# Kernel optimization log

Measured on AMD Instinct MI355X. Metric: run time of the kernel, lower is better.

## Reference

```python
import jax, jax.numpy as jnp
import numpy as np

B, S, D = 2, 4096, 1024
H, HD = 16, 64
CF = 0.5
K = int(S * CF)          # top_k tokens routed through the block
HIDDEN = 4 * D
EPS = 1e-5
SCALE = 1.0 / float(np.sqrt(HD))


def rmsnorm(x, w):
    return x * jax.lax.rsqrt(jnp.mean(x * x, axis=-1, keepdims=True) + EPS) * w


def rope(x, cos, sin):
    # x: [B,K,H,HD]; cos/sin: [K, HD//2]
    x1, x2 = x[..., ::2], x[..., 1::2]
    c = cos[None, :, None, :]
    s = sin[None, :, None, :]
    r1 = x1 * c - x2 * s
    r2 = x1 * s + x2 * c
    return jnp.stack([r1, r2], axis=-1).reshape(x.shape)


def block(x, mask, cos, sin, attn_norm, wq, wk, wv, wo, ffn_norm, w1, w2, w3):
    # Llama-style decoder block on the routed subset x: [B,K,D]
    b, k, _ = x.shape
    xn = rmsnorm(x, attn_norm)
    q = (xn @ wq).reshape(b, k, H, HD)
    kk = (xn @ wk).reshape(b, k, H, HD)
    v = (xn @ wv).reshape(b, k, H, HD)
    q = rope(q, cos, sin)
    kk = rope(kk, cos, sin)
    scores = jnp.einsum('bqhd,bkhd->bhqk', q, kk) * SCALE
    scores = jnp.where(mask[None, None], scores, jnp.finfo(scores.dtype).min)
    attn = jax.nn.softmax(scores, axis=-1)
    o = jnp.einsum('bhqk,bkhd->bqhd', attn, v).reshape(b, k, D)
    h = x + o @ wo
    hn = rmsnorm(h, ffn_norm)
    return h + (jax.nn.silu(hn @ w1) * (hn @ w3)) @ w2


def setup_inputs() -> dict:
    key = jax.random.key(0)
    ks = jax.random.split(key, 10)
    sc = 0.02
    inv = 1.0 / (10000.0 ** (np.arange(0, HD, 2, dtype=np.float32) / HD))
    ang = np.outer(np.arange(K, dtype=np.float32), inv)  # [K, HD//2]
    return {
        'x': jax.random.normal(ks[0], (B, S, D), jnp.float32),
        'mask': jnp.tril(jnp.ones((K, K), dtype=bool)),
        'freqs_cos': jnp.asarray(np.cos(ang)),
        'freqs_sin': jnp.asarray(np.sin(ang)),
        'w_router': jax.random.normal(ks[1], (D, 1), jnp.float32) * sc,
        'attn_norm': jnp.ones((D,), jnp.float32),
        'wq': jax.random.normal(ks[2], (D, D), jnp.float32) * sc,
        'wk': jax.random.normal(ks[3], (D, D), jnp.float32) * sc,
        'wv': jax.random.normal(ks[4], (D, D), jnp.float32) * sc,
        'wo': jax.random.normal(ks[5], (D, D), jnp.float32) * sc,
        'ffn_norm': jnp.ones((D,), jnp.float32),
        'w1': jax.random.normal(ks[6], (D, HIDDEN), jnp.float32) * sc,
        'w2': jax.random.normal(ks[7], (HIDDEN, D), jnp.float32) * sc,
        'w3': jax.random.normal(ks[8], (D, HIDDEN), jnp.float32) * sc,
    }


def reference(x, mask, freqs_cos, freqs_sin, w_router, attn_norm, wq, wk, wv, wo, ffn_norm, w1, w2, w3):
    b = x.shape[0]
    router_logits = (x @ w_router)[..., 0]            # [B,S]
    vals, idx = jax.lax.top_k(router_logits, K)       # [B,K]
    order = jnp.argsort(idx, axis=1)                  # torch.sort of token_index
    sel = jnp.take_along_axis(idx, order, axis=1)     # sorted selected positions
    token_w = jax.nn.softmax(vals, axis=1)            # softmax over topk weights
    r_weights = jnp.take_along_axis(token_w, order, axis=1)  # [B,K]
    filtered_x = jnp.take_along_axis(x, sel[:, :, None], axis=1)  # [B,K,D]
    x_out = block(filtered_x, mask, freqs_cos, freqs_sin, attn_norm,
                  wq, wk, wv, wo, ffn_norm, w1, w2, w3)
    xw_out = r_weights[:, :, None] * x_out
    # scatter_add back into the residual stream
    out = x.at[jnp.arange(b)[:, None], sel, :].add(xw_out)
    return out
```

## Files before the change

### kernel.cpp

```cpp
#include <hip/hip_runtime.h>
#include <cstdint>
#include <cstddef>

typedef unsigned short u16;
typedef __bf16 bf16x8 __attribute__((ext_vector_type(8)));
typedef short s16x4 __attribute__((ext_vector_type(4)));
typedef float f32x4 __attribute__((ext_vector_type(4)));

#define SCALE_Q_LOG2E 0.18033688011112042f

static __device__ __forceinline__ float b2f(u16 u){ return __uint_as_float(((unsigned)u)<<16); }
static __device__ __forceinline__ u16 f2b(float f){
  unsigned u = __float_as_uint(f);
  return (u16)((u + 0x7fffu + ((u>>16)&1u)) >> 16);
}
static __device__ __forceinline__ void gload_lds16(const void* g, void* l){
  auto gp = reinterpret_cast<__attribute__((address_space(1))) uint32_t*>(reinterpret_cast<uintptr_t>(g));
  auto lp = reinterpret_cast<__attribute__((address_space(3))) uint32_t*>(reinterpret_cast<uintptr_t>(l));
  __builtin_amdgcn_global_load_lds(gp, lp, 16, 0, 0);
}
static __device__ __forceinline__ f32x4 mfma16bf(s16x4 a, s16x4 b, f32x4 c){
#if __has_builtin(__builtin_amdgcn_mfma_f32_16x16x16bf16_1k)
  return __builtin_amdgcn_mfma_f32_16x16x16bf16_1k(a, b, c, 0, 0, 0);
#else
  f32x4 d = c;
  asm volatile("v_mfma_f32_16x16x16_bf16 %0, %1, %2, %0" : "+v"(d) : "v"(a), "v"(b));
  return d;
#endif
}

__global__ __launch_bounds__(256) void prep_weights(
    const float* __restrict__ wq, const float* __restrict__ wk,
    const float* __restrict__ wv, const float* __restrict__ wo,
    const float* __restrict__ w1, const float* __restrict__ w3,
    const float* __restrict__ w2,
    u16* __restrict__ WqkvT, u16* __restrict__ WoT,
    u16* __restrict__ W13T, u16* __restrict__ W2T){
  __shared__ float tile[32][33];
  int bx = blockIdx.x;
  const float* in; u16* out; int R, C, rowmap, tcol, trow;
  if (bx < 4096){
    int wsel = bx>>10, tid = bx&1023;
    in = (wsel==0)?wq:(wsel==1)?wk:(wsel==2)?wv:wo;
    out = (wsel<3) ? (WqkvT + (size_t)wsel*1024*1024) : WoT;
    R=1024; C=1024; rowmap=0; tcol=tid&31; trow=tid>>5;
  } else if (bx < 12288){
    int wsel=(bx-4096)>>12, tid=(bx-4096)&4095;
    in = wsel ? w3 : w1; out = W13T; R=1024; C=4096; rowmap=1+wsel;
    tcol=tid&127; trow=tid>>7;
  } else {
    int tid = bx-12288;
    in = w2; out = W2T; R=4096; C=1024; rowmap=0;
    tcol=tid&31; trow=tid>>5;
  }
  int t=threadIdx.x, tx=t&31, ty=t>>5;
  int c0=tcol*32, r0=trow*32;
  #pragma unroll
  for (int i=0;i<4;i++) tile[ty+i*8][tx] = in[(size_t)(r0+ty+i*8)*C + c0+tx];
  __syncthreads();
  #pragma unroll
  for (int i=0;i<4;i++){
    int c = c0+ty+i*8;
    int orow = c;
    if (rowmap==1) orow = (c>>4)*32 + (c&15);
    else if (rowmap==2) orow = (c>>4)*32 + 16 + (c&15);
    out[(size_t)orow*R + r0+tx] = f2b(tile[tx][ty+i*8]);
  }
}

__global__ __launch_bounds__(256) void transpose_bf16(const u16* __restrict__ in, u16* __restrict__ out,
                                                      int R, int C){
  __shared__ u16 tile[32][33];
  size_t zoff = (size_t)blockIdx.z * R * C;
  const u16* ip = in + zoff;
  u16* op = out + zoff;
  int tx = threadIdx.x, ty = threadIdx.y;
  int c0 = blockIdx.x*32, r0 = blockIdx.y*32;
  #pragma unroll
  for (int i=0;i<4;i++) tile[ty+i*8][tx] = ip[(size_t)(r0+ty+i*8)*C + c0+tx];
  __syncthreads();
  #pragma unroll
  for (int i=0;i<4;i++) op[(size_t)(c0+ty+i*8)*R + r0+tx] = tile[tx][ty+i*8];
}

__global__ __launch_bounds__(256) void router_kernel(const float* __restrict__ x, const float* __restrict__ wr,
                                                     float* __restrict__ logits){
  int row = blockIdx.x*4 + (threadIdx.x>>6);
  int l = threadIdx.x & 63;
  const float4* xr = (const float4*)(x + (size_t)row*1024) + l;
  const float4* wp = (const float4*)wr + l;
  float acc = 0.f;
  #pragma unroll
  for (int c=0;c<4;c++){
    float4 xv = xr[c*64];
    float4 wv = wp[c*64];
    acc += xv.x*wv.x + xv.y*wv.y + xv.z*wv.z + xv.w*wv.w;
  }
  #pragma unroll
  for (int m=1;m<64;m<<=1) acc += __shfl_xor(acc, m, 64);
  if (l==0) logits[row] = acc;
}

static __device__ __forceinline__ unsigned mapkey(float f){
  unsigned u = __float_as_uint(f);
  return (u & 0x80000000u) ? ~u : (u | 0x80000000u);
}
static __device__ unsigned blk_scan_excl(unsigned cnt, unsigned* swav){
  int t = threadIdx.x; int l = t&63, w = t>>6;
  unsigned v = cnt;
  #pragma unroll
  for (int off=1; off<64; off<<=1){
    unsigned n = __shfl_up(v, off, 64);
    if (l >= off) v += n;
  }
  __syncthreads();
  if (l==63) swav[w] = v;
  __syncthreads();
  if (t==0){ unsigned c=0; for (int i=0;i<16;i++){ unsigned tmp=swav[i]; swav[i]=c; c+=tmp; } }
  __syncthreads();
  return swav[w] + v - cnt;
}
__global__ __launch_bounds__(1024) void topk_kernel(const float* __restrict__ logits,
        int* __restrict__ sel, float* __restrict__ rw, int* __restrict__ inv){
  int b = blockIdx.x, t = threadIdx.x;
  int l = t&63, w = t>>6;
  __shared__ float vals[4096];
  __shared__ unsigned hist[256];
  __shared__ unsigned swav[16];
  __shared__ float fwav[16];
  __shared__ unsigned sh_prefix, sh_remaining;
  const float* lgp = logits + b*4096;
  for (int i=t;i<4096;i+=1024) vals[i]=lgp[i];
  if (t==0){ sh_prefix=0u; sh_remaining=2048u; }
  __syncthreads();
  for (int level=0; level<4; level++){
    int shift = 24 - level*8;
    if (t<256) hist[t]=0u;
    __syncthreads();
    unsigned pfx = sh_prefix;
    for (int i=t;i<4096;i+=1024){
      unsigned key = mapkey(vals[i]);
      if (level==0 || (key >> (shift+8)) == pfx)
        atomicAdd(&hist[(key>>shift)&255u], 1u);
    }
    __syncthreads();
    if (t==0){
      unsigned rem = sh_remaining, cum=0u; unsigned bsel=0u;
      for (int bin=255; bin>=0; bin--){
        unsigned hc = hist[bin];
        if (cum + hc >= rem){ bsel=(unsigned)bin; break; }
        cum += hc;
      }
      sh_remaining = rem - cum;
      sh_prefix = (pfx<<8) | bsel;
    }
    __syncthreads();
  }
  unsigned T = sh_prefix;
  unsigned req = sh_remaining;
  int i0 = t*4;
  unsigned gt_[4], eq_[4], fl_[4]; float v_[4];
  #pragma unroll
  for (int j=0;j<4;j++){
    v_[j] = vals[i0+j];
    unsigned key = mapkey(v_[j]);
    gt_[j] = key > T ? 1u:0u;
    eq_[j] = key == T ? 1u:0u;
  }
  unsigned eqbase = blk_scan_excl(eq_[0]+eq_[1]+eq_[2]+eq_[3], swav);
  unsigned er = eqbase;
  #pragma unroll
  for (int j=0;j<4;j++){ fl_[j] = gt_[j] | (eq_[j] & (er < req ? 1u:0u)); er += eq_[j]; }
  unsigned pbase = blk_scan_excl(fl_[0]+fl_[1]+fl_[2]+fl_[3], swav);
  unsigned p = pbase;
  #pragma unroll
  for (int j=0;j<4;j++){
    int i = i0+j;
    if (fl_[j]){ sel[b*2048+(int)p]=i; inv[b*4096+i]=(int)p; p++; }
    else inv[b*4096+i] = -1;
  }
  float mx = fmaxf(fmaxf(v_[0],v_[1]), fmaxf(v_[2],v_[3]));
  #pragma unroll
  for (int m=1;m<64;m<<=1) mx = fmaxf(mx, __shfl_xor(mx,m,64));
  __syncthreads();
  if (l==0) fwav[w]=mx;
  __syncthreads();
  if (t==0){ float g=fwav[0]; for(int i=1;i<16;i++) g=fmaxf(g,fwav[i]); fwav[0]=g; }
  __syncthreads();
  float gm = fwav[0];
  float zz = 0.f;
  #pragma unroll
  for (int j=0;j<4;j++) if (fl_[j]) zz += expf(v_[j]-gm);
  #pragma unroll
  for (int m=1;m<64;m<<=1) zz += __shfl_xor(zz,m,64);
  __syncthreads();
  if (l==0) fwav[w]=zz;
  __syncthreads();
  if (t==0){ float s=0.f; for(int i=0;i<16;i++) s+=fwav[i]; fwav[0]=s; }
  __syncthreads();
  float Z = fwav[0];
  unsigned p2 = pbase;
  #pragma unroll
  for (int j=0;j<4;j++) if (fl_[j]){ rw[b*2048+(int)p2] = expf(v_[j]-gm)/Z; p2++; }
}

__global__ __launch_bounds__(256) void rmsnorm_kernel(const float* __restrict__ xin,
        const float* __restrict__ gamma, const int* __restrict__ sel,
        u16* __restrict__ xn){
  int r = blockIdx.x;
  int src = r;
  if (sel) src = (r>>11)*4096 + sel[r];
  const float* row = xin + (size_t)src*1024;
  int t = threadIdx.x, l = t&63, w = t>>6;
  int d0 = t*4;
  float4 xv = *(const float4*)(row + d0);
  float ss = xv.x*xv.x + xv.y*xv.y + xv.z*xv.z + xv.w*xv.w;
  #pragma unroll
  for (int m=1;m<64;m<<=1) ss += __shfl_xor(ss,m,64);
  __shared__ float red[4];
  if (l==0) red[w]=ss;
  __syncthreads();
  float tot = red[0]+red[1]+red[2]+red[3];
  float rms = rsqrtf(tot*(1.f/1024.f) + 1e-5f);
  float4 gv = *(const float4*)(gamma + d0);
  u16 o0=f2b(xv.x*rms*gv.x), o1=f2b(xv.y*rms*gv.y), o2=f2b(xv.z*rms*gv.z), o3=f2b(xv.w*rms*gv.w);
  uint2 ov; ov.x = (unsigned)o0 | ((unsigned)o1<<16); ov.y = (unsigned)o2 | ((unsigned)o3<<16);
  *(uint2*)(xn + (size_t)r*1024 + d0) = ov;
}

template<int BK>
static __device__ __forceinline__ int swz(int row, int blk){
  if constexpr (BK==64) return blk ^ (row&7);
  else                  return blk ^ ((row>>1)&3);
}

template<int BN, int BK, typename OT>
__global__ __launch_bounds__(256,2) void gemm_bt(const u16* __restrict__ A, const u16* __restrict__ Bt,
        OT* __restrict__ C, const float* __restrict__ resid, const int* __restrict__ sel,
        int M, int N, int Kd){
  __shared__ u16 As[128*BK];
  __shared__ u16 Bs[BN*BK];
  constexpr int NF = BN/32;
  constexpr int KK = BK/32;
  int t = threadIdx.x, w = t>>6, l = t&63, lg = l>>4, ln = l&15;
  int m0 = blockIdx.y*128, n0 = blockIdx.x*BN;
  int wm = (w&1)*64, wn = (w>>1)*(BN/2);
  f32x4 acc[4][NF] = {};
  for (int k0=0; k0<Kd; k0+=BK){
    __syncthreads();
    #pragma unroll
    for (int c=0;c<128*BK*2/4096;c++){
      int off = t*16 + c*4096;
      int row = off/(BK*2), pb = (off%(BK*2))>>4;
      gload_lds16(A + (size_t)(m0+row)*Kd + k0 + swz<BK>(row,pb)*8, &As[c*2048 + w*512]);
    }
    #pragma unroll
    for (int c=0;c<BN*BK*2/4096;c++){
      int off = t*16 + c*4096;
      int row = off/(BK*2), pb = (off%(BK*2))>>4;
      gload_lds16(Bt + (size_t)(n0+row)*Kd + k0 + swz<BK>(row,pb)*8, &Bs[c*2048 + w*512]);
    }
    __syncthreads();
    #pragma unroll
    for (int kk=0;kk<KK;kk++){
      bf16x8 af[4], bfv[NF];
      #pragma unroll
      for (int i=0;i<4;i++){
        int r = wm+i*16+ln;
        af[i] = *(const bf16x8*)&As[r*BK + swz<BK>(r, kk*4+lg)*8];
      }
      #pragma unroll
      for (int i=0;i<NF;i++){
        int r = wn+i*16+ln;
        bfv[i] = *(const bf16x8*)&Bs[r*BK + swz<BK>(r, kk*4+lg)*8];
      }
      #pragma unroll
      for (int mi=0;mi<4;mi++)
        #pragma unroll
        for (int ni=0;ni<NF;ni++)
          acc[mi][ni] = __builtin_amdgcn_mfma_f32_16x16x32_bf16(af[mi], bfv[ni], acc[mi][ni], 0,0,0);
    }
  }
  #pragma unroll
  for (int mi=0;mi<4;mi++){
    #pragma unroll
    for (int ni=0;ni<NF;ni++){
      #pragma unroll
      for (int r=0;r<4;r++){
        int row = m0+wm+mi*16+lg*4+r;
        int col = n0+wn+ni*16+ln;
        float v = acc[mi][ni][r];
        if (resid){
          size_t rrow = sel ? ((size_t)(row>>11)*4096 + sel[row]) : (size_t)row;
          v += resid[rrow*N + col];
        }
        if constexpr (sizeof(OT)==2) C[(size_t)row*N + col] = f2b(v);
        else                          C[(size_t)row*N + col] = v;
      }
    }
  }
}

__global__ __launch_bounds__(256,2) void gemm13(const u16* __restrict__ A, const u16* __restrict__ Bt,
        u16* __restrict__ g, int Kd){
  constexpr int BK = 64;
  __shared__ u16 As[128*BK];
  __shared__ u16 Bs[128*BK];
  int t = threadIdx.x, w = t>>6, l = t&63, lg = l>>4, ln = l&15;
  int m0 = blockIdx.y*128, n0 = blockIdx.x*128;
  int wm = (w&1)*64, wn = (w>>1)*64;
  f32x4 acc[4][4] = {};
  for (int k0=0; k0<Kd; k0+=BK){
    __syncthreads();
    #pragma unroll
    for (int c=0;c<4;c++){
      int off = t*16 + c*4096;
      int row = off/(BK*2), pb = (off%(BK*2))>>4;
      gload_lds16(A  + (size_t)(m0+row)*Kd + k0 + swz<BK>(row,pb)*8, &As[c*2048 + w*512]);
      gload_lds16(Bt + (size_t)(n0+row)*Kd + k0 + swz<BK>(row,pb)*8, &Bs[c*2048 + w*512]);
    }
    __syncthreads();
    #pragma unroll
    for (int kk=0;kk<2;kk++){
      bf16x8 af[4], bfv[4];
      #pragma unroll
      for (int i=0;i<4;i++){
        int ra = wm+i*16+ln, rb = wn+i*16+ln;
        af[i]  = *(const bf16x8*)&As[ra*BK + swz<BK>(ra, kk*4+lg)*8];
        bfv[i] = *(const bf16x8*)&Bs[rb*BK + swz<BK>(rb, kk*4+lg)*8];
      }
      #pragma unroll
      for (int mi=0;mi<4;mi++)
        #pragma unroll
        for (int ni=0;ni<4;ni++)
          acc[mi][ni] = __builtin_amdgcn_mfma_f32_16x16x32_bf16(af[mi], bfv[ni], acc[mi][ni], 0,0,0);
    }
  }
  int gbase = (n0+wn)>>1;
  #pragma unroll
  for (int mi=0;mi<4;mi++){
    #pragma unroll
    for (int p=0;p<2;p++){
      #pragma unroll
      for (int r=0;r<4;r++){
        int row = m0+wm+mi*16+lg*4+r;
        int col = gbase + p*16 + ln;
        float a1 = acc[mi][2*p][r], a3 = acc[mi][2*p+1][r];
        float s1 = a1 / (1.f + __expf(-a1));
        g[(size_t)row*4096 + col] = f2b(s1*a3);
      }
    }
  }
}

__global__ __launch_bounds__(256) void rope_kernel(const u16* __restrict__ QKV,
        const float* __restrict__ fcos, const float* __restrict__ fsin,
        u16* __restrict__ q_r, u16* __restrict__ k_r, u16* __restrict__ v_r){
  int row = blockIdx.x;
  int tok = row & 2047;
  int t = threadIdx.x;
  int d0 = t*4;
  int h = d0 >> 6, wd = d0 & 63, i0 = wd >> 1;
  const u16* base = QKV + (size_t)row*3072;
  size_t ob = (((size_t)(row>>11)*16 + h)*2048 + (size_t)tok)*64 + wd;
  float c0 = fcos[tok*32+i0],   s0 = fsin[tok*32+i0];
  float c1 = fcos[tok*32+i0+1], s1 = fsin[tok*32+i0+1];
  const u16* qp = base + d0;
  float x0=b2f(qp[0]), x1=b2f(qp[1]), x2=b2f(qp[2]), x3=b2f(qp[3]);
  q_r[ob]   = f2b((x0*c0-x1*s0)*SCALE_Q_LOG2E);
  q_r[ob+1] = f2b((x0*s0+x1*c0)*SCALE_Q_LOG2E);
  q_r[ob+2] = f2b((x2*c1-x3*s1)*SCALE_Q_LOG2E);
  q_r[ob+3] = f2b((x2*s1+x3*c1)*SCALE_Q_LOG2E);
  const u16* kp = base + 1024 + d0;
  x0=b2f(kp[0]); x1=b2f(kp[1]); x2=b2f(kp[2]); x3=b2f(kp[3]);
  k_r[ob]   = f2b(x0*c0-x1*s0);
  k_r[ob+1] = f2b(x0*s0+x1*c0);
  k_r[ob+2] = f2b(x2*c1-x3*s1);
  k_r[ob+3] = f2b(x2*s1+x3*c1);
  const u16* vp = base + 2048 + d0;
  v_r[ob]=vp[0]; v_r[ob+1]=vp[1]; v_r[ob+2]=vp[2]; v_r[ob+3]=vp[3];
}

static __device__ __forceinline__ void flash_tile(
    const u16* __restrict__ Ksb, const u16* __restrict__ Vsb,
    bf16x8 qf0, bf16x8 qf1, int k0, int q, bool diag,
    int lg, int ln, float& mi, float& li, f32x4* oaccT){
  f32x4 sv[4];
  #pragma unroll
  for (int ni=0;ni<4;ni++){
    bf16x8 kf0 = *(const bf16x8*)&Ksb[(ni*16+ln)*72 + lg*8];
    bf16x8 kf1 = *(const bf16x8*)&Ksb[(ni*16+ln)*72 + 32 + lg*8];
    f32x4 z = {};
    z = __builtin_amdgcn_mfma_f32_16x16x32_bf16(kf0, qf0, z, 0,0,0);
    z = __builtin_amdgcn_mfma_f32_16x16x32_bf16(kf1, qf1, z, 0,0,0);
    sv[ni] = z;
  }
  float rm = -1e30f;
  if (diag){
    #pragma unroll
    for (int ni=0;ni<4;ni++)
      #pragma unroll
      for (int r=0;r<4;r++){
        float xs = sv[ni][r];
        if (k0+ni*16+lg*4+r > q) xs = -1e30f;
        sv[ni][r] = xs;
        rm = fmaxf(rm, xs);
      }
  } else {
    #pragma unroll
    for (int ni=0;ni<4;ni++)
      #pragma unroll
      for (int r=0;r<4;r++) rm = fmaxf(rm, sv[ni][r]);
  }
  rm = fmaxf(rm, __shfl_xor(rm, 16, 64));
  rm = fmaxf(rm, __shfl_xor(rm, 32, 64));
  float mn = fmaxf(mi, rm);
  float alpha = exp2f(mi - mn);
  float ls = 0.f;
  s16x4 pf[4];
  #pragma unroll
  for (int ni=0;ni<4;ni++){
    float p0 = exp2f(sv[ni][0]-mn);
    float p1 = exp2f(sv[ni][1]-mn);
    float p2 = exp2f(sv[ni][2]-mn);
    float p3 = exp2f(sv[ni][3]-mn);
    ls += (p0+p1)+(p2+p3);
    s16x4 pp;
    pp[0]=(short)f2b(p0); pp[1]=(short)f2b(p1); pp[2]=(short)f2b(p2); pp[3]=(short)f2b(p3);
    pf[ni]=pp;
  }
  ls += __shfl_xor(ls, 16, 64);
  ls += __shfl_xor(ls, 32, 64);
  li = li*alpha + ls;
  mi = mn;
  #pragma unroll
  for (int dt=0; dt<4; dt++){
    f32x4 oo = oaccT[dt];
    oo[0]*=alpha; oo[1]*=alpha; oo[2]*=alpha; oo[3]*=alpha;
    #pragma unroll
    for (int ni=0;ni<4;ni++){
      s16x4 vf = *(const s16x4*)&Vsb[(dt*16+ln)*72 + ni*16 + lg*4];
      oo = mfma16bf(vf, pf[ni], oo);
    }
    oaccT[dt] = oo;
  }
}

__global__ __launch_bounds__(256,2) void flash_kernel(const u16* __restrict__ q_r,
        const u16* __restrict__ k_r, const u16* __restrict__ v_t, u16* __restrict__ o){
  const int S = 2048;
  int pr = blockIdx.x, bh = blockIdx.y;
  int b = bh>>4, h = bh&15;
  int t = threadIdx.x, w = t>>6, l = t&63, lg = l>>4, ln = l&15;
  __shared__ u16 Ks[2][64*72];
  __shared__ u16 Vs[2][64*72];
  const u16* qb = q_r + (size_t)bh*S*64;
  const u16* kb = k_r + (size_t)bh*S*64;
  const u16* vb = v_t + (size_t)bh*64*S;
  int rr = t>>2, p16 = (t&3)*16;
  int qlo = pr, qhi = 31-pr;
  int qAr = qlo*64 + w*16 + ln;
  int qBr = qhi*64 + w*16 + ln;
  bf16x8 qA0 = *(const bf16x8*)(qb + (size_t)qAr*64 + lg*8);
  bf16x8 qA1 = *(const bf16x8*)(qb + (size_t)qAr*64 + 32 + lg*8);
  bf16x8 qB0 = *(const bf16x8*)(qb + (size_t)qBr*64 + lg*8);
  bf16x8 qB1 = *(const bf16x8*)(qb + (size_t)qBr*64 + 32 + lg*8);
  f32x4 oA[4] = {}, oB[4] = {};
  float miA=-1e30f, liA=0.f, miB=-1e30f, liB=0.f;
  {
    *(bf16x8*)&Ks[0][rr*72+p16]   = *(const bf16x8*)(kb + (size_t)rr*64 + p16);
    *(bf16x8*)&Ks[0][rr*72+p16+8] = *(const bf16x8*)(kb + (size_t)rr*64 + p16 + 8);
    *(bf16x8*)&Vs[0][rr*72+p16]   = *(const bf16x8*)(vb + (size_t)rr*S + p16);
    *(bf16x8*)&Vs[0][rr*72+p16+8] = *(const bf16x8*)(vb + (size_t)rr*S + p16 + 8);
  }
  __syncthreads();
  for (int kv=0; kv<=qhi; kv++){
    int cur = kv&1;
    int k0 = kv*64;
    bool hasnext = kv < qhi;
    bf16x8 nk0, nk1, nv0, nv1;
    if (hasnext){
      int kn = k0 + 64;
      nk0 = *(const bf16x8*)(kb + (size_t)(kn+rr)*64 + p16);
      nk1 = *(const bf16x8*)(kb + (size_t)(kn+rr)*64 + p16 + 8);
      nv0 = *(const bf16x8*)(vb + (size_t)rr*S + kn + p16);
      nv1 = *(const bf16x8*)(vb + (size_t)rr*S + kn + p16 + 8);
    }
    if (kv <= qlo)
      flash_tile(Ks[cur], Vs[cur], qA0, qA1, k0, qAr, kv==qlo, lg, ln, miA, liA, oA);
    flash_tile(Ks[cur], Vs[cur], qB0, qB1, k0, qBr, kv==qhi, lg, ln, miB, liB, oB);
    if (hasnext){
      int nb = cur^1;
      *(bf16x8*)&Ks[nb][rr*72+p16]   = nk0;
      *(bf16x8*)&Ks[nb][rr*72+p16+8] = nk1;
      *(bf16x8*)&Vs[nb][rr*72+p16]   = nv0;
      *(bf16x8*)&Vs[nb][rr*72+p16+8] = nv1;
    }
    __syncthreads();
  }
  {
    u16* ob = o + ((size_t)(b*S+qAr))*1024 + h*64 + lg*4;
    #pragma unroll
    for (int dt=0; dt<4; dt++){
      u16 a0=f2b(oA[dt][0]/liA), a1=f2b(oA[dt][1]/liA);
      u16 a2=f2b(oA[dt][2]/liA), a3=f2b(oA[dt][3]/liA);
      uint2 pv; pv.x = (unsigned)a0 | ((unsigned)a1<<16); pv.y = (unsigned)a2 | ((unsigned)a3<<16);
      *(uint2*)(ob + dt*16) = pv;
    }
  }
  {
    u16* ob = o + ((size_t)(b*S+qBr))*1024 + h*64 + lg*4;
    #pragma unroll
    for (int dt=0; dt<4; dt++){
      u16 a0=f2b(oB[dt][0]/liB), a1=f2b(oB[dt][1]/liB);
      u16 a2=f2b(oB[dt][2]/liB), a3=f2b(oB[dt][3]/liB);
      uint2 pv; pv.x = (unsigned)a0 | ((unsigned)a1<<16); pv.y = (unsigned)a2 | ((unsigned)a3<<16);
      *(uint2*)(ob + dt*16) = pv;
    }
  }
}

__global__ __launch_bounds__(256) void final_kernel(const float* __restrict__ x, const float* __restrict__ h,
        const u16* __restrict__ y, const int* __restrict__ inv, const float* __restrict__ rw,
        float* __restrict__ out){
  int row = blockIdx.x;
  int b = row>>12;
  int t = threadIdx.x, d0 = t*4;
  float4 xv = *(const float4*)(x + (size_t)row*1024 + d0);
  float4* op = (float4*)(out + (size_t)row*1024 + d0);
  int j = inv[row];
  if (j < 0){ *op = xv; return; }
  int fr = b*2048 + j;
  float wgt = rw[fr];
  float4 hv = *(const float4*)(h + (size_t)fr*1024 + d0);
  uint2 yv = *(const uint2*)(y + (size_t)fr*1024 + d0);
  float y0=b2f((u16)(yv.x&0xffffu)), y1=b2f((u16)(yv.x>>16)), y2=b2f((u16)(yv.y&0xffffu)), y3=b2f((u16)(yv.y>>16));
  float4 ov;
  ov.x = xv.x + wgt*(hv.x + y0);
  ov.y = xv.y + wgt*(hv.y + y1);
  ov.z = xv.z + wgt*(hv.z + y2);
  ov.w = xv.w + wgt*(hv.w + y3);
  *op = ov;
}

extern "C" void kernel_launch(void* const* d_in, const int* in_sizes, int n_in,
                              void* d_out, int out_size, void* d_ws, size_t ws_size,
                              hipStream_t stream) {
  (void)in_sizes; (void)n_in; (void)out_size; (void)ws_size;
  const float* x     = (const float*)d_in[0];
  const float* fcos  = (const float*)d_in[2];
  const float* fsin  = (const float*)d_in[3];
  const float* wr    = (const float*)d_in[4];
  const float* anorm = (const float*)d_in[5];
  const float* wq    = (const float*)d_in[6];
  const float* wk    = (const float*)d_in[7];
  const float* wv    = (const float*)d_in[8];
  const float* wo    = (const float*)d_in[9];
  const float* fnorm = (const float*)d_in[10];
  const float* w1    = (const float*)d_in[11];
  const float* w2    = (const float*)d_in[12];
  const float* w3    = (const float*)d_in[13];
  float* out = (float*)d_out;

  char* W = (char*)d_ws;
  const size_t MB = 1024*1024;
  u16* WqkvT = (u16*)(W + 0);
  u16* WoT   = (u16*)(W + 6*MB);
  u16* W13T  = (u16*)(W + 8*MB);
  u16* W2T   = (u16*)(W + 24*MB);
  u16* xn    = (u16*)(W + 32*MB);
  u16* QKV   = (u16*)(W + 40*MB);
  u16* q_r   = (u16*)(W + 64*MB);
  u16* k_r   = (u16*)(W + 72*MB);
  u16* v_r   = (u16*)(W + 80*MB);
  u16* v_t   = (u16*)(W + 88*MB);
  u16* attno = (u16*)(W + 96*MB);
  float* hbuf= (float*)(W + 104*MB);
  u16* hn    = (u16*)(W + 120*MB);
  u16* g     = (u16*)(W + 128*MB);
  u16* ybuf  = (u16*)(W + 32*MB);
  float* logits = (float*)(W + 160*MB);
  int*   sel    = (int*)(W + 160*MB + 64*1024);
  float* rw     = (float*)(W + 160*MB + 96*1024);
  int*   inv    = (int*)(W + 160*MB + 128*1024);

  prep_weights<<<16384, 256, 0, stream>>>(wq, wk, wv, wo, w1, w3, w2, WqkvT, WoT, W13T, W2T);
  router_kernel<<<2048, 256, 0, stream>>>(x, wr, logits);
  topk_kernel<<<2, 1024, 0, stream>>>(logits, sel, rw, inv);
  rmsnorm_kernel<<<4096, 256, 0, stream>>>(x, anorm, sel, xn);
  gemm_bt<128,64,u16><<<dim3(24,32), 256, 0, stream>>>(xn, WqkvT, QKV, nullptr, nullptr, 4096, 3072, 1024);
  rope_kernel<<<4096, 256, 0, stream>>>(QKV, fcos, fsin, q_r, k_r, v_r);
  transpose_bf16<<<dim3(2,64,32), dim3(32,8), 0, stream>>>(v_r, v_t, 2048, 64);
  flash_kernel<<<dim3(16,32), 256, 0, stream>>>(q_r, k_r, v_t, attno);
  gemm_bt<64,64,float><<<dim3(16,32), 256, 0, stream>>>(attno, WoT, hbuf, x, sel, 4096, 1024, 1024);
  rmsnorm_kernel<<<4096, 256, 0, stream>>>(hbuf, fnorm, nullptr, hn);
  gemm13<<<dim3(64,32), 256, 0, stream>>>(hn, W13T, g, 1024);
  gemm_bt<64,64,u16><<<dim3(16,32), 256, 0, stream>>>(g, W2T, ybuf, nullptr, nullptr, 4096, 1024, 4096);
  final_kernel<<<8192, 256, 0, stream>>>(x, hbuf, ybuf, inv, rw, out);
}
```

Measured before the change: 489.4 us.

## Fuse router and output copy into prep kernel, fuse W2 GEMM epilogue scatter

The router logits and a full copy of x into the output are merged into the weight-prep kernel, which saves two launches. The W2 GEMM now applies the routing weight and residual in its epilogue and scatters straight into the output at the selected rows. This removes the bf16 ybuf round trip and the separate final kernel. The flash kernel also hoists its K/V LDS fragment loads so both query tiles share one set of registers, which raises register pressure. Correctness depends on the copy of x finishing before the scatter writes, which stream ordering guarantees.

```diff
diff --git a/kernel.cpp b/kernel.cpp
--- a/kernel.cpp
+++ b/kernel.cpp
@@ -29,42 +29,65 @@
 #endif
 }
 
-__global__ __launch_bounds__(256) void prep_weights(
+__global__ __launch_bounds__(256) void prep_kernel(
     const float* __restrict__ wq, const float* __restrict__ wk,
     const float* __restrict__ wv, const float* __restrict__ wo,
     const float* __restrict__ w1, const float* __restrict__ w3,
-    const float* __restrict__ w2,
+    const float* __restrict__ w2, const float* __restrict__ x,
+    const float* __restrict__ wr,
     u16* __restrict__ WqkvT, u16* __restrict__ WoT,
-    u16* __restrict__ W13T, u16* __restrict__ W2T){
+    u16* __restrict__ W13T, u16* __restrict__ W2T,
+    float* __restrict__ logits, float* __restrict__ out){
   __shared__ float tile[32][33];
   int bx = blockIdx.x;
-  const float* in; u16* out; int R, C, rowmap, tcol, trow;
-  if (bx < 4096){
-    int wsel = bx>>10, tid = bx&1023;
-    in = (wsel==0)?wq:(wsel==1)?wk:(wsel==2)?wv:wo;
-    out = (wsel<3) ? (WqkvT + (size_t)wsel*1024*1024) : WoT;
-    R=1024; C=1024; rowmap=0; tcol=tid&31; trow=tid>>5;
-  } else if (bx < 12288){
-    int wsel=(bx-4096)>>12, tid=(bx-4096)&4095;
-    in = wsel ? w3 : w1; out = W13T; R=1024; C=4096; rowmap=1+wsel;
-    tcol=tid&127; trow=tid>>7;
+  if (bx < 12288 || (bx >= 12288 && bx < 13312) || (bx>=13312 && bx<16384)){ }
+  if (bx < 16384){
+    const float* in; u16* outp; int R, C, rowmap, tcol, trow;
+    if (bx < 4096){
+      int wsel = bx>>10, tid = bx&1023;
+      in = (wsel==0)?wq:(wsel==1)?wk:(wsel==2)?wv:wo;
+      outp = (wsel<3) ? (WqkvT + (size_t)wsel*1024*1024) : WoT;
+      R=1024; C=1024; rowmap=0; tcol=tid&31; trow=tid>>5;
+    } else if (bx < 12288){
+      int wsel=(bx-4096)>>12, tid=(bx-4096)&4095;
+      in = wsel ? w3 : w1; outp = W13T; R=1024; C=4096; rowmap=1+wsel;
+      tcol=tid&127; trow=tid>>7;
+    } else {
+      int tid = bx-12288;
+      in = w2; outp = W2T; R=4096; C=1024; rowmap=0;
+      tcol=tid&31; trow=tid>>5;
+    }
+    int t=threadIdx.x, tx=t&31, ty=t>>5;
+    int c0=tcol*32, r0=trow*32;
+    #pragma unroll
+    for (int i=0;i<4;i++) tile[ty+i*8][tx] = in[(size_t)(r0+ty+i*8)*C + c0+tx];
+    __syncthreads();
+    #pragma unroll
+    for (int i=0;i<4;i++){
+      int c = c0+ty+i*8;
+      int orow = c;
+      if (rowmap==1) orow = (c>>4)*32 + (c&15);
+      else if (rowmap==2) orow = (c>>4)*32 + 16 + (c&15);
+      outp[(size_t)orow*R + r0+tx] = f2b(tile[tx][ty+i*8]);
+    }
+  } else if (bx < 18432){
+    int row = (bx-16384)*4 + (threadIdx.x>>6);
+    int l = threadIdx.x & 63;
+    const float4* xr = (const float4*)(x + (size_t)row*1024) + l;
+    const float4* wp = (const float4*)wr + l;
+    float acc = 0.f;
+    #pragma unroll
+    for (int c=0;c<4;c++){
+      float4 xv = xr[c*64];
+      float4 wv = wp[c*64];
+      acc += xv.x*wv.x + xv.y*wv.y + xv.z*wv.z + xv.w*wv.w;
+    }
+    #pragma unroll
+    for (int m=1;m<64;m<<=1) acc += __shfl_xor(acc, m, 64);
+    if (l==0) logits[row] = acc;
   } else {
-    int tid = bx-12288;
-    in = w2; out = W2T; R=4096; C=1024; rowmap=0;
-    tcol=tid&31; trow=tid>>5;
-  }
-  int t=threadIdx.x, tx=t&31, ty=t>>5;
-  int c0=tcol*32, r0=trow*32;
-  #pragma unroll
-  for (int i=0;i<4;i++) tile[ty+i*8][tx] = in[(size_t)(r0+ty+i*8)*C + c0+tx];
-  __syncthreads();
-  #pragma unroll
-  for (int i=0;i<4;i++){
-    int c = c0+ty+i*8;
-    int orow = c;
-    if (rowmap==1) orow = (c>>4)*32 + (c&15);
-    else if (rowmap==2) orow = (c>>4)*32 + 16 + (c&15);
-    out[(size_t)orow*R + r0+tx] = f2b(tile[tx][ty+i*8]);
+    size_t idx = ((size_t)(bx-18432)*256 + threadIdx.x)*4;
+    *(float4*)(out+idx) = *(const float4*)(x+idx);
   }
 }
 
@@ -81,24 +104,6 @@
   __syncthreads();
   #pragma unroll
   for (int i=0;i<4;i++) op[(size_t)(c0+ty+i*8)*R + r0+tx] = tile[tx][ty+i*8];
-}
-
-__global__ __launch_bounds__(256) void router_kernel(const float* __restrict__ x, const float* __restrict__ wr,
-                                                     float* __restrict__ logits){
-  int row = blockIdx.x*4 + (threadIdx.x>>6);
-  int l = threadIdx.x & 63;
-  const float4* xr = (const float4*)(x + (size_t)row*1024) + l;
-  const float4* wp = (const float4*)wr + l;
-  float acc = 0.f;
-  #pragma unroll
-  for (int c=0;c<4;c++){
-    float4 xv = xr[c*64];
-    float4 wv = wp[c*64];
-    acc += xv.x*wv.x + xv.y*wv.y + xv.z*wv.z + xv.w*wv.w;
-  }
-  #pragma unroll
-  for (int m=1;m<64;m<<=1) acc += __shfl_xor(acc, m, 64);
-  if (l==0) logits[row] = acc;
 }
 
 static __device__ __forceinline__ unsigned mapkey(float f){
@@ -296,6 +301,72 @@
         }
         if constexpr (sizeof(OT)==2) C[(size_t)row*N + col] = f2b(v);
         else                          C[(size_t)row*N + col] = v;
+      }
+    }
+  }
+}
+
+__global__ __launch_bounds__(256,2) void gemm_w2(const u16* __restrict__ A, const u16* __restrict__ Bt,
+        const float* __restrict__ x, const float* __restrict__ hbuf,
+        const int* __restrict__ sel, const float* __restrict__ rw,
+        float* __restrict__ out, int Kd){
+  constexpr int BN = 64, BK = 64;
+  __shared__ u16 As[128*BK];
+  __shared__ u16 Bs[BN*BK];
+  int t = threadIdx.x, w = t>>6, l = t&63, lg = l>>4, ln = l&15;
+  int m0 = blockIdx.y*128, n0 = blockIdx.x*BN;
+  int wm = (w&1)*64, wn = (w>>1)*(BN/2);
+  f32x4 acc[4][2] = {};
+  for (int k0=0; k0<Kd; k0+=BK){
+    __syncthreads();
+    #pragma unroll
+    for (int c=0;c<4;c++){
+      int off = t*16 + c*4096;
+      int row = off/(BK*2), pb = (off%(BK*2))>>4;
+      gload_lds16(A + (size_t)(m0+row)*Kd + k0 + swz<BK>(row,pb)*8, &As[c*2048 + w*512]);
+    }
+    #pragma unroll
+    for (int c=0;c<2;c++){
+      int off = t*16 + c*4096;
+      int row = off/(BK*2), pb = (off%(BK*2))>>4;
+      gload_lds16(Bt + (size_t)(n0+row)*Kd + k0 + swz<BK>(row,pb)*8, &Bs[c*2048 + w*512]);
+    }
+    __syncthreads();
+    #pragma unroll
+    for (int kk=0;kk<2;kk++){
+      bf16x8 af[4], bfv[2];
+      #pragma unroll
+      for (int i=0;i<4;i++){
+        int r = wm+i*16+ln;
+        af[i] = *(const bf16x8*)&As[r*BK + swz<BK>(r, kk*4+lg)*8];
+      }
+      #pragma unroll
+      for (int i=0;i<2;i++){
+        int r = wn+i*16+ln;
+        bfv[i] = *(const bf16x8*)&Bs[r*BK + swz<BK>(r, kk*4+lg)*8];
+      }
+      #pragma unroll
+      for (int mi=0;mi<4;mi++)
+        #pragma unroll
+        for (int ni=0;ni<2;ni++)
+          acc[mi][ni] = __builtin_amdgcn_mfma_f32_16x16x32_bf16(af[mi], bfv[ni], acc[mi][ni], 0,0,0);
+    }
+  }
+  #pragma unroll
+  for (int mi=0;mi<4;mi++){
+    int row0 = m0+wm+mi*16+lg*4;
+    #pragma unroll
+    for (int r=0;r<4;r++){
+      int row = row0+r;
+      int b = row>>11;
+      size_t srow = (size_t)b*4096 + sel[row];
+      float wgt = rw[row];
+      #pragma unroll
+      for (int ni=0;ni<2;ni++){
+        int col = n0+wn+ni*16+ln;
+        float y = acc[mi][ni][r];
+        float v = x[srow*1024 + col] + wgt*(hbuf[(size_t)row*1024 + col] + y);
+        out[srow*1024 + col] = v;
       }
     }
   }
@@ -382,17 +453,15 @@
 }
 
 static __device__ __forceinline__ void flash_tile(
-    const u16* __restrict__ Ksb, const u16* __restrict__ Vsb,
+    const bf16x8 (&kf)[4][2], const s16x4 (&vf)[4][4],
     bf16x8 qf0, bf16x8 qf1, int k0, int q, bool diag,
-    int lg, int ln, float& mi, float& li, f32x4* oaccT){
+    int lg, float& mi, float& li, f32x4* oaccT){
   f32x4 sv[4];
   #pragma unroll
   for (int ni=0;ni<4;ni++){
-    bf16x8 kf0 = *(const bf16x8*)&Ksb[(ni*16+ln)*72 + lg*8];
-    bf16x8 kf1 = *(const bf16x8*)&Ksb[(ni*16+ln)*72 + 32 + lg*8];
     f32x4 z = {};
-    z = __builtin_amdgcn_mfma_f32_16x16x32_bf16(kf0, qf0, z, 0,0,0);
-    z = __builtin_amdgcn_mfma_f32_16x16x32_bf16(kf1, qf1, z, 0,0,0);
+    z = __builtin_amdgcn_mfma_f32_16x16x32_bf16(kf[ni][0], qf0, z, 0,0,0);
+    z = __builtin_amdgcn_mfma_f32_16x16x32_bf16(kf[ni][1], qf1, z, 0,0,0);
     sv[ni] = z;
   }
   float rm = -1e30f;
@@ -438,10 +507,8 @@
     f32x4 oo = oaccT[dt];
     oo[0]*=alpha; oo[1]*=alpha; oo[2]*=alpha; oo[3]*=alpha;
     #pragma unroll
-    for (int ni=0;ni<4;ni++){
-      s16x4 vf = *(const s16x4*)&Vsb[(dt*16+ln)*72 + ni*16 + lg*4];
-      oo = mfma16bf(vf, pf[ni], oo);
-    }
+    for (int ni=0;ni<4;ni++)
+      oo = mfma16bf(vf[dt][ni], pf[ni], oo);
     oaccT[dt] = oo;
   }
 }
@@ -486,9 +553,20 @@
       nv0 = *(const bf16x8*)(vb + (size_t)rr*S + kn + p16);
       nv1 = *(const bf16x8*)(vb + (size_t)rr*S + kn + p16 + 8);
     }
+    bf16x8 kf[4][2]; s16x4 vf[4][4];
+    #pragma unroll
+    for (int ni=0;ni<4;ni++){
+      kf[ni][0] = *(const bf16x8*)&Ks[cur][(ni*16+ln)*72 + lg*8];
+      kf[ni][1] = *(const bf16x8*)&Ks[cur][(ni*16+ln)*72 + 32 + lg*8];
+    }
+    #pragma unroll
+    for (int dt=0;dt<4;dt++)
+      #pragma unroll
+      for (int ni=0;ni<4;ni++)
+        vf[dt][ni] = *(const s16x4*)&Vs[cur][(dt*16+ln)*72 + ni*16 + lg*4];
     if (kv <= qlo)
-      flash_tile(Ks[cur], Vs[cur], qA0, qA1, k0, qAr, kv==qlo, lg, ln, miA, liA, oA);
-    flash_tile(Ks[cur], Vs[cur], qB0, qB1, k0, qBr, kv==qhi, lg, ln, miB, liB, oB);
+      flash_tile(kf, vf, qA0, qA1, k0, qAr, kv==qlo, lg, miA, liA, oA);
+    flash_tile(kf, vf, qB0, qB1, k0, qBr, kv==qhi, lg, miB, liB, oB);
     if (hasnext){
       int nb = cur^1;
       *(bf16x8*)&Ks[nb][rr*72+p16]   = nk0;
@@ -518,29 +596,6 @@
       *(uint2*)(ob + dt*16) = pv;
     }
   }
-}
-
-__global__ __launch_bounds__(256) void final_kernel(const float* __restrict__ x, const float* __restrict__ h,
-        const u16* __restrict__ y, const int* __restrict__ inv, const float* __restrict__ rw,
-        float* __restrict__ out){
-  int row = blockIdx.x;
-  int b = row>>12;
-  int t = threadIdx.x, d0 = t*4;
-  float4 xv = *(const float4*)(x + (size_t)row*1024 + d0);
-  float4* op = (float4*)(out + (size_t)row*1024 + d0);
-  int j = inv[row];
-  if (j < 0){ *op = xv; return; }
-  int fr = b*2048 + j;
-  float wgt = rw[fr];
-  float4 hv = *(const float4*)(h + (size_t)fr*1024 + d0);
-  uint2 yv = *(const uint2*)(y + (size_t)fr*1024 + d0);
-  float y0=b2f((u16)(yv.x&0xffffu)), y1=b2f((u16)(yv.x>>16)), y2=b2f((u16)(yv.y&0xffffu)), y3=b2f((u16)(yv.y>>16));
-  float4 ov;
-  ov.x = xv.x + wgt*(hv.x + y0);
-  ov.y = xv.y + wgt*(hv.y + y1);
-  ov.z = xv.z + wgt*(hv.z + y2);
-  ov.w = xv.w + wgt*(hv.w + y3);
-  *op = ov;
 }
 
 extern "C" void kernel_launch(void* const* d_in, const int* in_sizes, int n_in,
@@ -578,15 +633,15 @@
   float* hbuf= (float*)(W + 104*MB);
   u16* hn    = (u16*)(W + 120*MB);
   u16* g     = (u16*)(W + 128*MB);
-  u16* ybuf  = (u16*)(W + 32*MB);
   float* logits = (float*)(W + 160*MB);
   int*   sel    = (int*)(W + 160*MB + 64*1024);
   float* rw     = (float*)(W + 160*MB + 96*1024);
   int*   inv    = (int*)(W + 160*MB + 128*1024);
-
-  prep_weights<<<16384, 256, 0, stream>>>(wq, wk, wv, wo, w1, w3, w2, WqkvT, WoT, W13T, W2T);
-  router_kernel<<<2048, 256, 0, stream>>>(x, wr, logits);
-  topk_kernel<<<2, 1024, 0, stream>>>(logits, sel, rw, inv);
+  (void)inv;
+
+  prep_kernel<<<26624, 256, 0, stream>>>(wq, wk, wv, wo, w1, w3, w2, x, wr,
+                                         WqkvT, WoT, W13T, W2T, logits, out);
+  topk_kernel<<<2, 1024, 0, stream>>>(logits, sel, rw, (int*)(W + 160*MB + 128*1024));
   rmsnorm_kernel<<<4096, 256, 0, stream>>>(x, anorm, sel, xn);
   gemm_bt<128,64,u16><<<dim3(24,32), 256, 0, stream>>>(xn, WqkvT, QKV, nullptr, nullptr, 4096, 3072, 1024);
   rope_kernel<<<4096, 256, 0, stream>>>(QKV, fcos, fsin, q_r, k_r, v_r);
@@ -595,6 +650,5 @@
   gemm_bt<64,64,float><<<dim3(16,32), 256, 0, stream>>>(attno, WoT, hbuf, x, sel, 4096, 1024, 1024);
   rmsnorm_kernel<<<4096, 256, 0, stream>>>(hbuf, fnorm, nullptr, hn);
   gemm13<<<dim3(64,32), 256, 0, stream>>>(hn, W13T, g, 1024);
-  gemm_bt<64,64,u16><<<dim3(16,32), 256, 0, stream>>>(g, W2T, ybuf, nullptr, nullptr, 4096, 1024, 4096);
-  final_kernel<<<8192, 256, 0, stream>>>(x, hbuf, ybuf, inv, rw, out);
-}
+  gemm_w2<<<dim3(16,32), 256, 0, stream>>>(g, W2T, x, hbuf, sel, rw, out, 4096);
+}
```

Result: no change. 491.6 us (+0.4%).
